# Optimization experiments

Measured on AMD Instinct MI355X. Metric: run time of the kernel, lower is better.

## Reference

```python
import jax, jax.numpy as jnp
import numpy as np

NUM_TAGS = 20000
H_DIM = 256
EPS = 1e-5


def _layernorm(x, g, b):
    mu = x.mean(-1, keepdims=True)
    var = ((x - mu) ** 2).mean(-1, keepdims=True)
    return (x - mu) * jax.lax.rsqrt(var + EPS) * g + b


def setup_inputs() -> dict:
    key = jax.random.key(0)
    ks = jax.random.split(key, 16)
    B, F, T = 64, 128, 16
    h4 = H_DIM * 4
    s = 0.02
    return {
        "tags": jax.random.randint(ks[0], (B, F, T), 0, NUM_TAGS),
        "feature_counts": jax.random.uniform(ks[1], (B,), jnp.float32) * 100.0,
        # tag_norm LayerNorm(num_tags)
        "ln_g": jnp.ones((NUM_TAGS,), jnp.float32),
        "ln_b": jnp.zeros((NUM_TAGS,), jnp.float32),
        # encoder: Linear(num_tags+1 -> 4h), GELU, LayerNorm(4h), MLP(4h->4h->h)
        "w1": jax.random.normal(ks[2], (NUM_TAGS + 1, h4), jnp.float32) * s,
        "b1": jnp.zeros((h4,), jnp.float32),
        "ln2_g": jnp.ones((h4,), jnp.float32),
        "ln2_b": jnp.zeros((h4,), jnp.float32),
        "we1": jax.random.normal(ks[3], (h4, h4), jnp.float32) * s,
        "be1": jnp.zeros((h4,), jnp.float32),
        "we2": jax.random.normal(ks[4], (h4, H_DIM), jnp.float32) * s,
        "be2": jnp.zeros((H_DIM,), jnp.float32),
        # decoder: MLP(h -> 4h -> num_tags+1)
        "wd1": jax.random.normal(ks[5], (H_DIM, h4), jnp.float32) * s,
        "bd1": jnp.zeros((h4,), jnp.float32),
        "wd2": jax.random.normal(ks[6], (h4, NUM_TAGS + 1), jnp.float32) * s,
        "bd2": jnp.zeros((NUM_TAGS + 1,), jnp.float32),
    }


def reference(tags, feature_counts, ln_g, ln_b, w1, b1, ln2_g, ln2_b,
              we1, be1, we2, be2, wd1, bd1, wd2, bd2):
    B, F, T = tags.shape
    # multi_hot.scatter_(2, tags, 1).clamp_(0,1): duplicates within a row collapse to 1
    bi = jnp.arange(B)[:, None, None]
    fi = jnp.arange(F)[None, :, None]
    multi_hot = jnp.zeros((B, F, NUM_TAGS), jnp.float32).at[bi, fi, tags].set(1.0)
    tile_tag_count = multi_hot.sum(axis=1)  # [B, num_tags]

    yn = _layernorm(tile_tag_count, ln_g, ln_b)
    y = jnp.concatenate([feature_counts[:, None] / 100.0, yn], axis=1)  # [B, num_tags+1]

    # encoder
    h = jax.nn.gelu(y @ w1 + b1, approximate=False)
    h = _layernorm(h, ln2_g, ln2_b)
    h = jax.nn.gelu(h @ we1 + be1, approximate=False)
    enc = h @ we2 + be2  # [B, h_dim]

    # decoder
    d = jax.nn.gelu(enc @ wd1 + bd1, approximate=False)
    dec = d @ wd2 + bd2  # [B, num_tags+1]
    return (y, enc, dec)
```

## Files before the change

### kernel.cpp

```cpp
#include <hip/hip_runtime.h>
#include <math.h>

#define NUM_TAGS 20000
#define BATCH 64
#define H4 1024
#define HD 256
#define NT1 20001

__device__ __forceinline__ float gelu_exact(float x) {
    return 0.5f * x * (1.0f + erff(x * 0.7071067811865476f));
}

struct F4 { float x, y, z, w; };

typedef const __attribute__((address_space(1))) void* gp_t;
typedef __attribute__((address_space(3))) void* lp_t;
__device__ __forceinline__ void async_ld4(const float* g, float* lds_base) {
    __builtin_amdgcn_global_load_lds((gp_t)g, (lp_t)lds_base, 4, 0, 0);
}
__device__ __forceinline__ void async_ld16(const float* g, float* lds_base) {
    __builtin_amdgcn_global_load_lds((gp_t)g, (lp_t)lds_base, 16, 0, 0);
}

__global__ __launch_bounds__(1024) void k_ln1_fused(const int* __restrict__ tags,
                                                    const float* __restrict__ fc,
                                                    const float* __restrict__ lng,
                                                    const float* __restrict__ lnb,
                                                    float* __restrict__ y) {
    __shared__ int hist[NUM_TAGS];
    __shared__ float ls[16], ls2[16], smu, srs;
    const int b = blockIdx.x, tid = threadIdx.x;

    for (int t = tid; t < NUM_TAGS; t += 1024) hist[t] = 0;
    __syncthreads();

    if (tid < 128) {
        const int* tp = tags + ((size_t)(b * 128 + tid) << 4);
        int t[16];
#pragma unroll
        for (int i = 0; i < 16; ++i) t[i] = tp[i];
#pragma unroll
        for (int i = 0; i < 16; ++i) {
            bool dup = false;
            for (int j = 0; j < i; ++j) dup = dup || (t[j] == t[i]);
            if (!dup) atomicAdd(&hist[t[i]], 1);
        }
    }
    __syncthreads();

    float s = 0.f, s2 = 0.f;
    for (int t = tid; t < NUM_TAGS; t += 1024) {
        float v = (float)hist[t];
        s += v; s2 += v * v;
    }
#pragma unroll
    for (int off = 32; off > 0; off >>= 1) {
        s  += __shfl_down(s, off);
        s2 += __shfl_down(s2, off);
    }
    int wave = tid >> 6;
    if ((tid & 63) == 0) { ls[wave] = s; ls2[wave] = s2; }
    __syncthreads();
    if (tid == 0) {
        float S = 0.f, S2 = 0.f;
#pragma unroll
        for (int i = 0; i < 16; ++i) { S += ls[i]; S2 += ls2[i]; }
        float mu = S / (float)NUM_TAGS;
        float var = S2 / (float)NUM_TAGS - mu * mu;
        smu = mu;
        srs = rsqrtf(var + 1e-5f);
    }
    __syncthreads();
    float mu = smu, rs = srs;

    float* yrow = y + (size_t)b * NT1;
    if (tid == 0) yrow[0] = fc[b] * 0.01f;
    for (int t = tid; t < NUM_TAGS; t += 1024) {
        float v = (float)hist[t];
        yrow[1 + t] = (v - mu) * rs * lng[t] + lnb[t];
    }
}

template <int PATH>
__global__ __launch_bounds__(256, 2) void k_gemm(const float* __restrict__ A, int lda,
                                                 const float* __restrict__ W, int ldw,
                                                 float* __restrict__ P,
                                                 int N, int kpb) {
    __shared__ __align__(16) float As[4][512];
    __shared__ __align__(16) float Ws[4][1024];
    const int tid = threadIdx.x;
    const int lane = tid & 63, wid = tid >> 6;
    const int tn = tid & 15, tb = tid >> 4;
    const int n0 = blockIdx.x * 128;
    const int kstart = blockIdx.y * kpb;
    const int nchunk = kpb >> 3;

    float acc[4][8];
#pragma unroll
    for (int i = 0; i < 4; ++i)
#pragma unroll
        for (int j = 0; j < 8; ++j) acc[i][j] = 0.f;

    auto issue = [&](int b, int c) {
        int k0 = kstart + c * 8;
#pragma unroll
        for (int j = 0; j < 2; ++j) {
            int d0 = j * 256 + wid * 64;
            int d = d0 + lane;
            int k4 = d >> 8, row = (d & 255) >> 2, klo = d & 3;
            async_ld4(A + (size_t)row * lda + k0 + k4 * 4 + klo, &As[b][d0]);
        }
        if (PATH == 0) {
            int kk = tid >> 5, c4 = tid & 31;
            async_ld16(W + (size_t)(k0 + kk) * ldw + n0 + c4 * 4, &Ws[b][wid * 256]);
        } else {
#pragma unroll
            for (int j = 0; j < 4; ++j) {
                int d = j * 256 + tid;
                int kk = d >> 7, cc = d & 127;
                async_ld4(W + (size_t)(k0 + kk) * ldw + min(n0 + cc, N - 1),
                          &Ws[b][j * 256 + wid * 64]);
            }
        }
    };

    issue(0, 0);
    if (nchunk > 1) issue(1, 1);

    for (int c = 0; c < nchunk; ++c) {
        if (c + 2 < nchunk) issue((c + 2) & 3, c + 2);
        int ahead = nchunk - 1 - c;
        if (PATH == 0) {
            if (ahead >= 2)      asm volatile("s_waitcnt vmcnt(6)"  ::: "memory");
            else if (ahead == 1) asm volatile("s_waitcnt vmcnt(3)"  ::: "memory");
            else                 asm volatile("s_waitcnt vmcnt(0)"  ::: "memory");
        } else {
            if (ahead >= 2)      asm volatile("s_waitcnt vmcnt(12)" ::: "memory");
            else if (ahead == 1) asm volatile("s_waitcnt vmcnt(6)"  ::: "memory");
            else                 asm volatile("s_waitcnt vmcnt(0)"  ::: "memory");
        }
        __builtin_amdgcn_s_barrier();
        asm volatile("" ::: "memory");

        const float* Ab = As[c & 3];
        const float* Wb = Ws[c & 3];
        __builtin_amdgcn_s_setprio(1);
#pragma unroll
        for (int k4 = 0; k4 < 2; ++k4) {
            float4 a4[4];
#pragma unroll
            for (int i = 0; i < 4; ++i)
                a4[i] = *(const float4*)&Ab[k4 * 256 + (tb * 4 + i) * 4];
#pragma unroll
            for (int kl = 0; kl < 4; ++kl) {
                const float4 w0 = *(const float4*)&Wb[(k4 * 4 + kl) * 128 + tn * 4];
                const float4 w1 = *(const float4*)&Wb[(k4 * 4 + kl) * 128 + 64 + tn * 4];
#pragma unroll
                for (int i = 0; i < 4; ++i) {
                    float av = (kl == 0) ? a4[i].x : (kl == 1) ? a4[i].y
                             : (kl == 2) ? a4[i].z : a4[i].w;
                    acc[i][0] = fmaf(av, w0.x, acc[i][0]);
                    acc[i][1] = fmaf(av, w0.y, acc[i][1]);
                    acc[i][2] = fmaf(av, w0.z, acc[i][2]);
                    acc[i][3] = fmaf(av, w0.w, acc[i][3]);
                    acc[i][4] = fmaf(av, w1.x, acc[i][4]);
                    acc[i][5] = fmaf(av, w1.y, acc[i][5]);
                    acc[i][6] = fmaf(av, w1.z, acc[i][6]);
                    acc[i][7] = fmaf(av, w1.w, acc[i][7]);
                }
            }
        }
        __builtin_amdgcn_s_setprio(0);
        asm volatile("" ::: "memory");
    }

    float* Pp = P + ((size_t)blockIdx.x * gridDim.y + blockIdx.y) * 8192;
#pragma unroll
    for (int i = 0; i < 4; ++i) {
        int row = tb * 4 + i;
        float4 v0 = {acc[i][0], acc[i][1], acc[i][2], acc[i][3]};
        float4 v1 = {acc[i][4], acc[i][5], acc[i][6], acc[i][7]};
        *(float4*)&Pp[row * 128 + tn * 4]      = v0;
        *(float4*)&Pp[row * 128 + 64 + tn * 4] = v1;
    }
}

template <bool GELU>
__global__ __launch_bounds__(256) void k_reduce(const float* __restrict__ P, int KS,
                                                const float* __restrict__ bias,
                                                float* __restrict__ out, int ldo, int N) {
    int b = blockIdx.y;
    int n = blockIdx.x * 256 + threadIdx.x;
    if (n >= N) return;
    int nb = n >> 7, col = n & 127;
    const float* p = P + (size_t)nb * KS * 8192 + b * 128 + col;
    float s0 = 0.f, s1 = 0.f, s2 = 0.f, s3 = 0.f;
    int k = 0;
    for (; k + 3 < KS; k += 4) {
        s0 += p[(size_t)(k + 0) * 8192];
        s1 += p[(size_t)(k + 1) * 8192];
        s2 += p[(size_t)(k + 2) * 8192];
        s3 += p[(size_t)(k + 3) * 8192];
    }
    for (; k < KS; ++k) s0 += p[(size_t)k * 8192];
    float s = (s0 + s1) + (s2 + s3) + bias[n];
    if (GELU) s = gelu_exact(s);
    out[(size_t)b * ldo + n] = s;
}

__global__ __launch_bounds__(1024) void k_red_ln2(const float* __restrict__ P, int KS,
                                                  const float* __restrict__ bias,
                                                  const float* __restrict__ r1row,
                                                  const float* __restrict__ fc,
                                                  const float* __restrict__ lng,
                                                  const float* __restrict__ lnb,
                                                  float* __restrict__ h2) {
    const int b = blockIdx.x, n = threadIdx.x;
    int nb = n >> 7, col = n & 127;
    const float* p = P + (size_t)nb * KS * 8192 + b * 128 + col;
    float s0 = 0.f, s1 = 0.f, s2v = 0.f, s3 = 0.f;
    int k = 0;
    for (; k + 3 < KS; k += 4) {
        s0  += p[(size_t)(k + 0) * 8192];
        s1  += p[(size_t)(k + 1) * 8192];
        s2v += p[(size_t)(k + 2) * 8192];
        s3  += p[(size_t)(k + 3) * 8192];
    }
    for (; k < KS; ++k) s0 += p[(size_t)k * 8192];
    float v = (s0 + s1) + (s2v + s3) + bias[n] + fc[b] * 0.01f * r1row[n];
    v = gelu_exact(v);

    float s = v, s2 = v * v;
#pragma unroll
    for (int off = 32; off > 0; off >>= 1) {
        s  += __shfl_down(s, off);
        s2 += __shfl_down(s2, off);
    }
    __shared__ float ls[16], ls2[16], smu, srs;
    int wave = n >> 6;
    if ((n & 63) == 0) { ls[wave] = s; ls2[wave] = s2; }
    __syncthreads();
    if (n == 0) {
        float S = 0.f, S2 = 0.f;
#pragma unroll
        for (int i = 0; i < 16; ++i) { S += ls[i]; S2 += ls2[i]; }
        float mu = S / (float)H4;
        float var = S2 / (float)H4 - mu * mu;
        smu = mu;
        srs = rsqrtf(var + 1e-5f);
    }
    __syncthreads();
    h2[(size_t)b * H4 + n] = (v - smu) * srs * lng[n] + lnb[n];
}

__global__ __launch_bounds__(256) void k_reduce_v4(const float* __restrict__ P, int KS,
                                                   const float* __restrict__ bias,
                                                   float* __restrict__ out, int ldo, int N) {
    int b = blockIdx.y;
    int n = (blockIdx.x * 256 + threadIdx.x) * 4;
    if (n >= N) return;
    int nb = n >> 7, col = n & 127;
    const float* p = P + (size_t)nb * KS * 8192 + b * 128 + col;
    if (n + 3 < N) {
        float sx = 0.f, sy = 0.f, sz = 0.f, sw = 0.f;
        for (int k = 0; k < KS; ++k) {
            float4 v = *(const float4*)&p[(size_t)k * 8192];
            sx += v.x; sy += v.y; sz += v.z; sw += v.w;
        }
        F4 bi = *(const F4*)&bias[n];
        F4 r = {sx + bi.x, sy + bi.y, sz + bi.z, sw + bi.w};
        *(F4*)&out[(size_t)b * ldo + n] = r;
    } else {
        for (int j = 0; n + j < N; ++j) {
            float s = 0.f;
            for (int k = 0; k < KS; ++k) s += p[(size_t)k * 8192 + j];
            out[(size_t)b * ldo + n + j] = s + bias[n + j];
        }
    }
}

extern "C" void kernel_launch(void* const* d_in, const int* in_sizes, int n_in,
                              void* d_out, int out_size, void* d_ws, size_t ws_size,
                              hipStream_t stream) {
    (void)in_sizes; (void)n_in; (void)out_size;
    const int*   tags  = (const int*)d_in[0];
    const float* fc    = (const float*)d_in[1];
    const float* ln_g  = (const float*)d_in[2];
    const float* ln_b  = (const float*)d_in[3];
    const float* w1    = (const float*)d_in[4];
    const float* b1    = (const float*)d_in[5];
    const float* ln2_g = (const float*)d_in[6];
    const float* ln2_b = (const float*)d_in[7];
    const float* we1   = (const float*)d_in[8];
    const float* be1   = (const float*)d_in[9];
    const float* we2   = (const float*)d_in[10];
    const float* be2   = (const float*)d_in[11];
    const float* wd1   = (const float*)d_in[12];
    const float* bd1   = (const float*)d_in[13];
    const float* wd2   = (const float*)d_in[14];
    const float* bd2   = (const float*)d_in[15];

    float* out = (float*)d_out;
    float* y   = out;
    float* enc = out + (size_t)BATCH * NT1;
    float* dec = enc + BATCH * HD;

    char* ws = (char*)d_ws;
    size_t off = 0;
    float* h2     = (float*)(ws + off); off += (size_t)BATCH * H4 * 4;
    float* g2     = (float*)(ws + off); off += (size_t)BATCH * H4 * 4;
    float* dd     = (float*)(ws + off); off += (size_t)BATCH * H4 * 4;
    float* arena  = (float*)(ws + off);
    size_t avail  = (ws_size > off) ? (ws_size - off) : 0;

    const size_t MB = 1024 * 1024;
    int KS5;
    if (avail >= 45 * MB)      { KS5 = 8; }
    else if (avail >= 33 * MB) { KS5 = 4; }
    else                       { KS5 = 2; }
    int kpb5 = H4 / KS5;

    k_ln1_fused<<<64, 1024, 0, stream>>>(tags, fc, ln_g, ln_b, y);

    k_gemm<0><<<dim3(8, 125), 256, 0, stream>>>(y + 1, NT1, w1 + H4, H4, arena, H4, 160);
    k_red_ln2<<<64, 1024, 0, stream>>>(arena, 125, b1, w1, fc, ln2_g, ln2_b, h2);

    k_gemm<0><<<dim3(8, 32), 256, 0, stream>>>(h2, H4, we1, H4, arena, H4, 32);
    k_reduce<true><<<dim3(4, 64), 256, 0, stream>>>(arena, 32, be1, g2, H4, H4);

    k_gemm<0><<<dim3(2, 64), 256, 0, stream>>>(g2, H4, we2, HD, arena, HD, 16);
    k_reduce<false><<<dim3(1, 64), 256, 0, stream>>>(arena, 64, be2, enc, HD, HD);

    k_gemm<0><<<dim3(8, 16), 256, 0, stream>>>(enc, HD, wd1, H4, arena, H4, 16);
    k_reduce<true><<<dim3(4, 64), 256, 0, stream>>>(arena, 16, bd1, dd, H4, H4);

    k_gemm<1><<<dim3(157, KS5), 256, 0, stream>>>(dd, H4, wd2, NT1, arena, NT1, kpb5);
    k_reduce_v4<<<dim3(20, 64), 256, 0, stream>>>(arena, KS5, bd2, dec, NT1, NT1);
}
```

Before: 314.9 us.

## Halve GEMM block threads, double per-thread rows, swizzle A tile, retune K-splits

```diff
diff --git a/kernel.cpp b/kernel.cpp
--- a/kernel.cpp
+++ b/kernel.cpp
@@ -81,48 +81,65 @@
     }
 }
 
-template <int PATH>
-__global__ __launch_bounds__(256, 2) void k_gemm(const float* __restrict__ A, int lda,
+template <int AMIS, int WMIS>
+__global__ __launch_bounds__(128, 2) void k_gemm(const float* __restrict__ A, int lda,
                                                  const float* __restrict__ W, int ldw,
                                                  float* __restrict__ P,
-                                                 int N, int kpb) {
+                                                 int N, int K, int kpb) {
     __shared__ __align__(16) float As[4][512];
     __shared__ __align__(16) float Ws[4][1024];
     const int tid = threadIdx.x;
-    const int lane = tid & 63, wid = tid >> 6;
+    const int wid = tid >> 6;
     const int tn = tid & 15, tb = tid >> 4;
+    const int tb3 = tb & 3;
     const int n0 = blockIdx.x * 128;
     const int kstart = blockIdx.y * kpb;
-    const int nchunk = kpb >> 3;
-
-    float acc[4][8];
-#pragma unroll
-    for (int i = 0; i < 4; ++i)
+    const int krem = K - kstart;
+    const int nchunk = (kpb < krem ? kpb : krem) >> 3;
+
+    float acc[8][8];
+#pragma unroll
+    for (int i = 0; i < 8; ++i)
 #pragma unroll
         for (int j = 0; j < 8; ++j) acc[i][j] = 0.f;
 
-    auto issue = [&](int b, int c) {
+    auto issue = [&](int buf, int c) {
         int k0 = kstart + c * 8;
-#pragma unroll
-        for (int j = 0; j < 2; ++j) {
-            int d0 = j * 256 + wid * 64;
-            int d = d0 + lane;
-            int k4 = d >> 8, row = (d & 255) >> 2, klo = d & 3;
-            async_ld4(A + (size_t)row * lda + k0 + k4 * 4 + klo, &As[b][d0]);
-        }
-        if (PATH == 0) {
-            int kk = tid >> 5, c4 = tid & 31;
-            async_ld16(W + (size_t)(k0 + kk) * ldw + n0 + c4 * 4, &Ws[b][wid * 256]);
+        if (AMIS) {
+#pragma unroll
+            for (int j = 0; j < 4; ++j) {
+                int qd = j * 128 + tid;
+                int q = qd >> 2, klo = qd & 3;
+                int g = q ^ ((q >> 3) & 3);
+                int row = g & 63, k4 = g >> 6;
+                async_ld4(A + (size_t)row * lda + k0 + k4 * 4 + klo,
+                          &As[buf][j * 128 + wid * 64]);
+            }
         } else {
-#pragma unroll
-            for (int j = 0; j < 4; ++j) {
-                int d = j * 256 + tid;
-                int kk = d >> 7, cc = d & 127;
+            int g = tid ^ ((tid >> 3) & 3);
+            int row = g & 63, k4 = g >> 6;
+            async_ld16(A + (size_t)row * lda + k0 + k4 * 4, &As[buf][wid * 256]);
+        }
+        if (WMIS) {
+#pragma unroll
+            for (int j = 0; j < 8; ++j) {
+                int qd = j * 128 + tid;
+                int kk = qd >> 7, cc = qd & 127;
                 async_ld4(W + (size_t)(k0 + kk) * ldw + min(n0 + cc, N - 1),
-                          &Ws[b][j * 256 + wid * 64]);
+                          &Ws[buf][j * 128 + wid * 64]);
             }
+        } else {
+#pragma unroll
+            for (int j = 0; j < 2; ++j) {
+                int q = j * 128 + tid;
+                int kk = q >> 5, c4 = q & 31;
+                async_ld16(W + (size_t)(k0 + kk) * ldw + n0 + c4 * 4,
+                           &Ws[buf][j * 512 + wid * 256]);
+            }
         }
     };
+
+    const int L = (AMIS ? 4 : 1) + (WMIS ? 8 : 2);
 
     issue(0, 0);
     if (nchunk > 1) issue(1, 1);
@@ -130,14 +147,16 @@
     for (int c = 0; c < nchunk; ++c) {
         if (c + 2 < nchunk) issue((c + 2) & 3, c + 2);
         int ahead = nchunk - 1 - c;
-        if (PATH == 0) {
-            if (ahead >= 2)      asm volatile("s_waitcnt vmcnt(6)"  ::: "memory");
-            else if (ahead == 1) asm volatile("s_waitcnt vmcnt(3)"  ::: "memory");
-            else                 asm volatile("s_waitcnt vmcnt(0)"  ::: "memory");
+        if (ahead >= 2) {
+            if (L == 6)       asm volatile("s_waitcnt vmcnt(12)" ::: "memory");
+            else if (L == 3)  asm volatile("s_waitcnt vmcnt(6)"  ::: "memory");
+            else              asm volatile("s_waitcnt vmcnt(18)" ::: "memory");
+        } else if (ahead == 1) {
+            if (L == 6)       asm volatile("s_waitcnt vmcnt(6)"  ::: "memory");
+            else if (L == 3)  asm volatile("s_waitcnt vmcnt(3)"  ::: "memory");
+            else              asm volatile("s_waitcnt vmcnt(9)"  ::: "memory");
         } else {
-            if (ahead >= 2)      asm volatile("s_waitcnt vmcnt(12)" ::: "memory");
-            else if (ahead == 1) asm volatile("s_waitcnt vmcnt(6)"  ::: "memory");
-            else                 asm volatile("s_waitcnt vmcnt(0)"  ::: "memory");
+            asm volatile("s_waitcnt vmcnt(0)" ::: "memory");
         }
         __builtin_amdgcn_s_barrier();
         asm volatile("" ::: "memory");
@@ -147,16 +166,16 @@
         __builtin_amdgcn_s_setprio(1);
 #pragma unroll
         for (int k4 = 0; k4 < 2; ++k4) {
-            float4 a4[4];
-#pragma unroll
-            for (int i = 0; i < 4; ++i)
-                a4[i] = *(const float4*)&Ab[k4 * 256 + (tb * 4 + i) * 4];
+            float4 a4[8];
+#pragma unroll
+            for (int i = 0; i < 8; ++i)
+                a4[i] = *(const float4*)&Ab[k4 * 256 + tb * 32 + ((i ^ tb3) << 2)];
 #pragma unroll
             for (int kl = 0; kl < 4; ++kl) {
                 const float4 w0 = *(const float4*)&Wb[(k4 * 4 + kl) * 128 + tn * 4];
                 const float4 w1 = *(const float4*)&Wb[(k4 * 4 + kl) * 128 + 64 + tn * 4];
 #pragma unroll
-                for (int i = 0; i < 4; ++i) {
+                for (int i = 0; i < 8; ++i) {
                     float av = (kl == 0) ? a4[i].x : (kl == 1) ? a4[i].y
                              : (kl == 2) ? a4[i].z : a4[i].w;
                     acc[i][0] = fmaf(av, w0.x, acc[i][0]);
@@ -176,8 +195,8 @@
 
     float* Pp = P + ((size_t)blockIdx.x * gridDim.y + blockIdx.y) * 8192;
 #pragma unroll
-    for (int i = 0; i < 4; ++i) {
-        int row = tb * 4 + i;
+    for (int i = 0; i < 8; ++i) {
+        int row = tb * 8 + i;
         float4 v0 = {acc[i][0], acc[i][1], acc[i][2], acc[i][3]};
         float4 v1 = {acc[i][4], acc[i][5], acc[i][6], acc[i][7]};
         *(float4*)&Pp[row * 128 + tn * 4]      = v0;
@@ -314,26 +333,29 @@
     size_t avail  = (ws_size > off) ? (ws_size - off) : 0;
 
     const size_t MB = 1024 * 1024;
-    int KS5;
-    if (avail >= 45 * MB)      { KS5 = 8; }
-    else if (avail >= 33 * MB) { KS5 = 4; }
-    else                       { KS5 = 2; }
+    int kpb1, KS5;
+    if (avail >= 45 * MB)      { kpb1 = 128; KS5 = 8; }
+    else if (avail >= 33 * MB) { kpb1 = 256; KS5 = 4; }
+    else                       { kpb1 = 320; KS5 = 2; }
+    int KS1  = (20000 + kpb1 - 1) / kpb1;
     int kpb5 = H4 / KS5;
 
     k_ln1_fused<<<64, 1024, 0, stream>>>(tags, fc, ln_g, ln_b, y);
 
-    k_gemm<0><<<dim3(8, 125), 256, 0, stream>>>(y + 1, NT1, w1 + H4, H4, arena, H4, 160);
-    k_red_ln2<<<64, 1024, 0, stream>>>(arena, 125, b1, w1, fc, ln2_g, ln2_b, h2);
-
-    k_gemm<0><<<dim3(8, 32), 256, 0, stream>>>(h2, H4, we1, H4, arena, H4, 32);
-    k_reduce<true><<<dim3(4, 64), 256, 0, stream>>>(arena, 32, be1, g2, H4, H4);
-
-    k_gemm<0><<<dim3(2, 64), 256, 0, stream>>>(g2, H4, we2, HD, arena, HD, 16);
+    k_gemm<1, 0><<<dim3(8, KS1), 128, 0, stream>>>(y + 1, NT1, w1 + H4, H4,
+                                                   arena, H4, 20000, kpb1);
+    k_red_ln2<<<64, 1024, 0, stream>>>(arena, KS1, b1, w1, fc, ln2_g, ln2_b, h2);
+
+    k_gemm<0, 0><<<dim3(8, 64), 128, 0, stream>>>(h2, H4, we1, H4, arena, H4, 1024, 16);
+    k_reduce<true><<<dim3(4, 64), 256, 0, stream>>>(arena, 64, be1, g2, H4, H4);
+
+    k_gemm<0, 0><<<dim3(2, 64), 128, 0, stream>>>(g2, H4, we2, HD, arena, HD, 1024, 16);
     k_reduce<false><<<dim3(1, 64), 256, 0, stream>>>(arena, 64, be2, enc, HD, HD);
 
-    k_gemm<0><<<dim3(8, 16), 256, 0, stream>>>(enc, HD, wd1, H4, arena, H4, 16);
+    k_gemm<0, 0><<<dim3(8, 16), 128, 0, stream>>>(enc, HD, wd1, H4, arena, H4, 256, 16);
     k_reduce<true><<<dim3(4, 64), 256, 0, stream>>>(arena, 16, bd1, dd, H4, H4);
 
-    k_gemm<1><<<dim3(157, KS5), 256, 0, stream>>>(dd, H4, wd2, NT1, arena, NT1, kpb5);
+    k_gemm<0, 1><<<dim3(157, KS5), 128, 0, stream>>>(dd, H4, wd2, NT1,
+                                                     arena, NT1, H4, kpb5);
     k_reduce_v4<<<dim3(20, 64), 256, 0, stream>>>(arena, KS5, bd2, dec, NT1, NT1);
 }
```

After: 362.4 us. 1.15x slower.

## Drop split-K for mid and decoder GEMMs, fuse bias into epilogue

Applied to the files above, without the earlier changes.

```diff
diff --git a/kernel.cpp b/kernel.cpp
--- a/kernel.cpp
+++ b/kernel.cpp
@@ -81,11 +81,12 @@
     }
 }
 
-template <int PATH>
+template <int PATH, int DIRECT>
 __global__ __launch_bounds__(256, 2) void k_gemm(const float* __restrict__ A, int lda,
                                                  const float* __restrict__ W, int ldw,
                                                  float* __restrict__ P,
-                                                 int N, int kpb) {
+                                                 int N, int kpb,
+                                                 const float* __restrict__ bias) {
     __shared__ __align__(16) float As[4][512];
     __shared__ __align__(16) float Ws[4][1024];
     const int tid = threadIdx.x;
@@ -174,38 +175,33 @@
         asm volatile("" ::: "memory");
     }
 
-    float* Pp = P + ((size_t)blockIdx.x * gridDim.y + blockIdx.y) * 8192;
-#pragma unroll
-    for (int i = 0; i < 4; ++i) {
-        int row = tb * 4 + i;
-        float4 v0 = {acc[i][0], acc[i][1], acc[i][2], acc[i][3]};
-        float4 v1 = {acc[i][4], acc[i][5], acc[i][6], acc[i][7]};
-        *(float4*)&Pp[row * 128 + tn * 4]      = v0;
-        *(float4*)&Pp[row * 128 + 64 + tn * 4] = v1;
-    }
-}
-
-template <bool GELU>
-__global__ __launch_bounds__(256) void k_reduce(const float* __restrict__ P, int KS,
-                                                const float* __restrict__ bias,
-                                                float* __restrict__ out, int ldo, int N) {
-    int b = blockIdx.y;
-    int n = blockIdx.x * 256 + threadIdx.x;
-    if (n >= N) return;
-    int nb = n >> 7, col = n & 127;
-    const float* p = P + (size_t)nb * KS * 8192 + b * 128 + col;
-    float s0 = 0.f, s1 = 0.f, s2 = 0.f, s3 = 0.f;
-    int k = 0;
-    for (; k + 3 < KS; k += 4) {
-        s0 += p[(size_t)(k + 0) * 8192];
-        s1 += p[(size_t)(k + 1) * 8192];
-        s2 += p[(size_t)(k + 2) * 8192];
-        s3 += p[(size_t)(k + 3) * 8192];
-    }
-    for (; k < KS; ++k) s0 += p[(size_t)k * 8192];
-    float s = (s0 + s1) + (s2 + s3) + bias[n];
-    if (GELU) s = gelu_exact(s);
-    out[(size_t)b * ldo + n] = s;
+    if (DIRECT) {
+#pragma unroll
+        for (int i = 0; i < 4; ++i) {
+            int row = tb * 4 + i;
+            float* crow = P + (size_t)row * N;
+#pragma unroll
+            for (int jj = 0; jj < 4; ++jj) {
+                int cn = n0 + tn * 4 + jj;
+                if (cn < N) crow[cn] = acc[i][jj] + bias[cn];
+            }
+#pragma unroll
+            for (int jj = 0; jj < 4; ++jj) {
+                int cn = n0 + 64 + tn * 4 + jj;
+                if (cn < N) crow[cn] = acc[i][4 + jj] + bias[cn];
+            }
+        }
+    } else {
+        float* Pp = P + ((size_t)blockIdx.x * gridDim.y + blockIdx.y) * 8192;
+#pragma unroll
+        for (int i = 0; i < 4; ++i) {
+            int row = tb * 4 + i;
+            float4 v0 = {acc[i][0], acc[i][1], acc[i][2], acc[i][3]};
+            float4 v1 = {acc[i][4], acc[i][5], acc[i][6], acc[i][7]};
+            *(float4*)&Pp[row * 128 + tn * 4]      = v0;
+            *(float4*)&Pp[row * 128 + 64 + tn * 4] = v1;
+        }
+    }
 }
 
 __global__ __launch_bounds__(1024) void k_red_ln2(const float* __restrict__ P, int KS,
@@ -253,30 +249,39 @@
     h2[(size_t)b * H4 + n] = (v - smu) * srs * lng[n] + lnb[n];
 }
 
-__global__ __launch_bounds__(256) void k_reduce_v4(const float* __restrict__ P, int KS,
-                                                   const float* __restrict__ bias,
-                                                   float* __restrict__ out, int ldo, int N) {
-    int b = blockIdx.y;
-    int n = (blockIdx.x * 256 + threadIdx.x) * 4;
-    if (n >= N) return;
-    int nb = n >> 7, col = n & 127;
-    const float* p = P + (size_t)nb * KS * 8192 + b * 128 + col;
-    if (n + 3 < N) {
-        float sx = 0.f, sy = 0.f, sz = 0.f, sw = 0.f;
-        for (int k = 0; k < KS; ++k) {
-            float4 v = *(const float4*)&p[(size_t)k * 8192];
-            sx += v.x; sy += v.y; sz += v.z; sw += v.w;
-        }
-        F4 bi = *(const F4*)&bias[n];
-        F4 r = {sx + bi.x, sy + bi.y, sz + bi.z, sw + bi.w};
-        *(F4*)&out[(size_t)b * ldo + n] = r;
-    } else {
-        for (int j = 0; n + j < N; ++j) {
-            float s = 0.f;
-            for (int k = 0; k < KS; ++k) s += p[(size_t)k * 8192 + j];
-            out[(size_t)b * ldo + n + j] = s + bias[n + j];
-        }
-    }
+template <bool GELU>
+__global__ __launch_bounds__(256) void k_mid(const float* __restrict__ A, int K,
+                                             const float* __restrict__ W, int N,
+                                             const float* __restrict__ bias,
+                                             float* __restrict__ out, int ldo) {
+    const int row = blockIdx.y;
+    const int c = blockIdx.x * 256 + threadIdx.x;
+    const float* Arow = A + (size_t)row * K;
+    const float* Wc = W + c;
+    float acc0 = 0.f, acc1 = 0.f;
+    for (int k0 = 0; k0 < K; k0 += 8) {
+        float4 a0 = *(const float4*)&Arow[k0];
+        float4 a1 = *(const float4*)&Arow[k0 + 4];
+        float w0 = Wc[(size_t)(k0 + 0) * N];
+        float w1 = Wc[(size_t)(k0 + 1) * N];
+        float w2 = Wc[(size_t)(k0 + 2) * N];
+        float w3 = Wc[(size_t)(k0 + 3) * N];
+        float w4 = Wc[(size_t)(k0 + 4) * N];
+        float w5 = Wc[(size_t)(k0 + 5) * N];
+        float w6 = Wc[(size_t)(k0 + 6) * N];
+        float w7 = Wc[(size_t)(k0 + 7) * N];
+        acc0 = fmaf(a0.x, w0, acc0);
+        acc1 = fmaf(a0.y, w1, acc1);
+        acc0 = fmaf(a0.z, w2, acc0);
+        acc1 = fmaf(a0.w, w3, acc1);
+        acc0 = fmaf(a1.x, w4, acc0);
+        acc1 = fmaf(a1.y, w5, acc1);
+        acc0 = fmaf(a1.z, w6, acc0);
+        acc1 = fmaf(a1.w, w7, acc1);
+    }
+    float v = acc0 + acc1 + bias[c];
+    if (GELU) v = gelu_exact(v);
+    out[(size_t)row * ldo + c] = v;
 }
 
 extern "C" void kernel_launch(void* const* d_in, const int* in_sizes, int n_in,
@@ -314,26 +319,20 @@
     size_t avail  = (ws_size > off) ? (ws_size - off) : 0;
 
     const size_t MB = 1024 * 1024;
-    int KS5;
-    if (avail >= 45 * MB)      { KS5 = 8; }
-    else if (avail >= 33 * MB) { KS5 = 4; }
-    else                       { KS5 = 2; }
-    int kpb5 = H4 / KS5;
+    int kpb1, KS1;
+    if (avail >= 33 * MB) { kpb1 = 160; KS1 = 125; }
+    else                  { kpb1 = 400; KS1 = 50;  }
 
     k_ln1_fused<<<64, 1024, 0, stream>>>(tags, fc, ln_g, ln_b, y);
 
-    k_gemm<0><<<dim3(8, 125), 256, 0, stream>>>(y + 1, NT1, w1 + H4, H4, arena, H4, 160);
-    k_red_ln2<<<64, 1024, 0, stream>>>(arena, 125, b1, w1, fc, ln2_g, ln2_b, h2);
-
-    k_gemm<0><<<dim3(8, 32), 256, 0, stream>>>(h2, H4, we1, H4, arena, H4, 32);
-    k_reduce<true><<<dim3(4, 64), 256, 0, stream>>>(arena, 32, be1, g2, H4, H4);
-
-    k_gemm<0><<<dim3(2, 64), 256, 0, stream>>>(g2, H4, we2, HD, arena, HD, 16);
-    k_reduce<false><<<dim3(1, 64), 256, 0, stream>>>(arena, 64, be2, enc, HD, HD);
-
-    k_gemm<0><<<dim3(8, 16), 256, 0, stream>>>(enc, HD, wd1, H4, arena, H4, 16);
-    k_reduce<true><<<dim3(4, 64), 256, 0, stream>>>(arena, 16, bd1, dd, H4, H4);
-
-    k_gemm<1><<<dim3(157, KS5), 256, 0, stream>>>(dd, H4, wd2, NT1, arena, NT1, kpb5);
-    k_reduce_v4<<<dim3(20, 64), 256, 0, stream>>>(arena, KS5, bd2, dec, NT1, NT1);
-}
+    k_gemm<1, 0><<<dim3(8, KS1), 256, 0, stream>>>(y + 1, NT1, w1 + H4, H4,
+                                                   arena, H4, kpb1, nullptr);
+    k_red_ln2<<<64, 1024, 0, stream>>>(arena, KS1, b1, w1, fc, ln2_g, ln2_b, h2);
+
+    k_mid<true><<<dim3(4, 64), 256, 0, stream>>>(h2, H4, we1, H4, be1, g2, H4);
+    k_mid<false><<<dim3(1, 64), 256, 0, stream>>>(g2, H4, we2, HD, be2, enc, HD);
+    k_mid<true><<<dim3(4, 64), 256, 0, stream>>>(enc, HD, wd1, H4, bd1, dd, H4);
+
+    k_gemm<1, 1><<<dim3(157, 1), 256, 0, stream>>>(dd, H4, wd2, NT1,
+                                                   dec, NT1, H4, bd2);
+}
```

Result: slower. 512.1 us (+62.6%).
